# Kernel optimization log

Measured on AMD Instinct MI355X. Metric: run time of the kernel, lower is better.

Reference implementation:

```python
import jax, jax.numpy as jnp
import numpy as np

N = 100000          # nodes
E = 1200000         # edges
IN_DIM = 128
HID = 64
NUM_CLASSES = 5
NUM_GRAPHS = 128


def setup_inputs() -> dict:
    key = jax.random.key(0)
    ks = jax.random.split(key, 12)
    x = jax.random.normal(ks[0], (N, IN_DIM), dtype=jnp.float32)
    edge_index = jax.random.randint(ks[1], (2, E), 0, N, dtype=jnp.int64)
    batch = jnp.sort(jax.random.randint(ks[2], (N,), 0, NUM_GRAPHS, dtype=jnp.int64))
    def glorot(k, shape):
        lim = np.sqrt(6.0 / (shape[0] + shape[1]))
        return jax.random.uniform(k, shape, jnp.float32, -lim, lim)
    W1 = glorot(ks[3], (IN_DIM, HID)); b1 = jnp.zeros((HID,), jnp.float32)
    W2 = glorot(ks[4], (HID, HID));    b2 = jnp.zeros((HID,), jnp.float32)
    W3 = glorot(ks[5], (HID, HID));    b3 = jnp.zeros((HID,), jnp.float32)
    Wc = glorot(ks[6], (HID, NUM_CLASSES)); bc = jnp.zeros((NUM_CLASSES,), jnp.float32)
    return {"x": x, "edge_index": edge_index, "batch": batch,
            "W1": W1, "b1": b1, "W2": W2, "b2": b2, "W3": W3, "b3": b3,
            "Wc": Wc, "bc": bc}


def _gcn_norm(edge_index, n_nodes):
    # PyG GCNConv: add self-loops, symmetric normalization D^-1/2 (A+I) D^-1/2
    loop = jnp.arange(n_nodes, dtype=edge_index.dtype)
    src = jnp.concatenate([edge_index[0], loop])  # [E+N]
    dst = jnp.concatenate([edge_index[1], loop])
    deg = jax.ops.segment_sum(jnp.ones_like(dst, dtype=jnp.float32), dst,
                              num_segments=n_nodes)
    dinv = jnp.where(deg > 0, jax.lax.rsqrt(deg), 0.0)
    norm = dinv[src] * dinv[dst]                   # [E+N]
    return src, dst, norm


def _gcn_conv(x, src, dst, norm, W, b, n_nodes):
    h = x @ W                                      # [N, out]
    msg = h[src] * norm[:, None]                   # gather + scale
    agg = jax.ops.segment_sum(msg, dst, num_segments=n_nodes)  # scatter-add
    return agg + b


def reference(x, edge_index, batch, W1, b1, W2, b2, W3, b3, Wc, bc):
    src, dst, norm = _gcn_norm(edge_index, N)
    h = jax.nn.relu(_gcn_conv(x, src, dst, norm, W1, b1, N))
    h = jax.nn.relu(_gcn_conv(h, src, dst, norm, W2, b2, N))
    h = jax.nn.relu(_gcn_conv(h, src, dst, norm, W3, b3, N))
    # global_mean_pool over batch ids
    sums = jax.ops.segment_sum(h, batch, num_segments=NUM_GRAPHS)
    counts = jax.ops.segment_sum(jnp.ones((N,), jnp.float32), batch,
                                 num_segments=NUM_GRAPHS)
    pooled = sums / jnp.maximum(counts, 1.0)[:, None]  # [G, HID]
    return pooled @ Wc + bc                             # [G, num_classes]
```

## Files before the change

### kernel.cpp

```cpp
#include <hip/hip_runtime.h>
#include <hip/hip_bf16.h>

#define NN 100000
#define NE 1200000
#define IND 128
#define HID 64
#define NC 5
#define NG 128
#define NB 391
#define GB 1172
#define G1 3125

typedef float v2f __attribute__((ext_vector_type(2)));

static __device__ __forceinline__ float bf2f(unsigned short u) {
    union { unsigned int i; float f; } x;
    x.i = (unsigned int)u << 16;
    return x.f;
}
static __device__ __forceinline__ unsigned short f2bf(float f) {
    union { float f; unsigned int i; } x;
    x.f = f;
    unsigned int r = (x.i + 0x7fffu + ((x.i >> 16) & 1u)) >> 16;
    return (unsigned short)r;
}
static __device__ __forceinline__ unsigned short f2fp8x2(float a, float b) {
    int p = __builtin_amdgcn_cvt_pk_fp8_f32(a, b, 0, false);
    return (unsigned short)(p & 0xffff);
}
static __device__ __forceinline__ void fp8acc(unsigned int u, float& a0, float& a1, float& a2, float& a3) {
    v2f lo = __builtin_amdgcn_cvt_pk_f32_fp8(u, false);
    v2f hi = __builtin_amdgcn_cvt_pk_f32_fp8(u, true);
    a0 += lo.x; a1 += lo.y; a2 += hi.x; a3 += hi.y;
}

__global__ __launch_bounds__(256) void k_hist(const int* __restrict__ dst, int* __restrict__ cnt,
                                              int* __restrict__ rank) {
    int e = blockIdx.x * 256 + threadIdx.x;
    if (e < NE) rank[e] = atomicAdd(&cnt[dst[e]], 1);
}

__global__ __launch_bounds__(256) void k_scan1(const int* __restrict__ cnt, int* __restrict__ exc,
                                               int* __restrict__ bsum, float* __restrict__ dinv) {
    __shared__ int lds[256];
    int tid = threadIdx.x;
    int i = blockIdx.x * 256 + tid;
    int v = (i < NN) ? cnt[i] : 0;
    lds[tid] = v;
    __syncthreads();
    for (int off = 1; off < 256; off <<= 1) {
        int t = (tid >= off) ? lds[tid - off] : 0;
        __syncthreads();
        lds[tid] += t;
        __syncthreads();
    }
    if (i < NN) {
        exc[i] = lds[tid] - v;
        dinv[i] = rsqrtf((float)v + 1.0f);
    }
    if (tid == 255) bsum[blockIdx.x] = lds[255];
}

__global__ __launch_bounds__(256) void k_scan23(const int* __restrict__ exc, const int* __restrict__ bsum,
                                                int* __restrict__ row_ptr) {
    __shared__ int lds[256];
    int tid = threadIdx.x;
    int me = blockIdx.x;
    int v = 0;
    if (tid < me) v = bsum[tid];
    if (tid + 256 < me) v += bsum[tid + 256];
    lds[tid] = v;
    __syncthreads();
    for (int off = 128; off > 0; off >>= 1) {
        if (tid < off) lds[tid] += lds[tid + off];
        __syncthreads();
    }
    int base = lds[0];
    int i = me * 256 + tid;
    if (i < NN) row_ptr[i] = exc[i] + base;
    if (i == 0) row_ptr[NN] = NE;
}

__global__ __launch_bounds__(256) void k_fused1(
    const float* __restrict__ X, const float* __restrict__ W,
    const float* __restrict__ dinv, unsigned short* __restrict__ out_f8,
    const int* __restrict__ src, const int* __restrict__ dst,
    const int* __restrict__ row_ptr, const int* __restrict__ rank,
    int* __restrict__ src_sorted,
    const int* __restrict__ batch, int* __restrict__ start)
{
    __shared__ float lds[IND * HID + 32 * IND];
    int tid = threadIdx.x;

    if (blockIdx.x < GB) {
        int t = blockIdx.x * 256 + tid;
        const int T = GB * 256;
#pragma unroll
        for (int u = 0; u < 4; ++u) {
            int e = t + u * T;
            if (e < NE) src_sorted[row_ptr[dst[e]] + rank[e]] = src[e];
        }
        return;
    }
    if (blockIdx.x >= GB + G1) {
        int i = (blockIdx.x - GB - G1) * 256 + tid;
        if (i >= NN) return;
        int b = batch[i];
        if (i == 0) {
            for (int g = 0; g <= b; ++g) start[g] = 0;
        } else {
            int p = batch[i - 1];
            for (int g = p + 1; g <= b; ++g) start[g] = i;
        }
        if (i == NN - 1) {
            for (int g = b + 1; g <= NG; ++g) start[g] = NN;
        }
        return;
    }

    float* Wl = lds;
    float* xl = lds + IND * HID;
    int n0 = (blockIdx.x - GB) * 32;
    int c = tid & 31;
    int s = tid >> 5;

    {
        const float4* Wg = (const float4*)W;
        float4* Wl4 = (float4*)Wl;
#pragma unroll
        for (int i = 0; i < IND * 16 / 256; ++i) Wl4[i * 256 + tid] = Wg[i * 256 + tid];
    }
    {
        const float4* Xg = (const float4*)X;
        float4* xl4 = (float4*)xl;
        const float4 z = {0.f, 0.f, 0.f, 0.f};
#pragma unroll
        for (int i = 0; i < 32 * IND / 4 / 256; ++i) {
            int idx = i * 256 + tid;
            int node = n0 + idx / (IND / 4);
            xl4[idx] = (node < NN) ? Xg[(size_t)n0 * (IND / 4) + idx] : z;
        }
    }
    __syncthreads();

    float acc[4][2];
#pragma unroll
    for (int r = 0; r < 4; ++r) { acc[r][0] = 0.f; acc[r][1] = 0.f; }

#pragma unroll 4
    for (int k0 = 0; k0 < IND; k0 += 4) {
        float4 xv[4];
#pragma unroll
        for (int r = 0; r < 4; ++r) xv[r] = *(const float4*)&xl[(s * 4 + r) * IND + k0];
#pragma unroll
        for (int kk = 0; kk < 4; ++kk) {
            float w0 = Wl[(k0 + kk) * HID + 2 * c];
            float w1 = Wl[(k0 + kk) * HID + 2 * c + 1];
#pragma unroll
            for (int r = 0; r < 4; ++r) {
                float xe = (kk == 0) ? xv[r].x : (kk == 1) ? xv[r].y : (kk == 2) ? xv[r].z : xv[r].w;
                acc[r][0] = fmaf(xe, w0, acc[r][0]);
                acc[r][1] = fmaf(xe, w1, acc[r][1]);
            }
        }
    }

#pragma unroll
    for (int r = 0; r < 4; ++r) {
        int n = n0 + s * 4 + r;
        if (n < NN) {
            float dn = dinv[n];
            out_f8[(size_t)n * 32 + c] = f2fp8x2(acc[r][0] * dn, acc[r][1] * dn);
        }
    }
}

__global__ __launch_bounds__(256) void k_aggregate(const unsigned int* __restrict__ hW8,
                                                   const int* __restrict__ srcs,
                                                   const int* __restrict__ row_ptr,
                                                   const float* __restrict__ dinv,
                                                   const float* __restrict__ b,
                                                   unsigned int* __restrict__ outb) {
    int tid = threadIdx.x;
    int lane = tid & 63;
    int grp = lane >> 4;
    int li = lane & 15;
    int n = blockIdx.x * 4 + (tid >> 6);

    float a0 = 0.f, a1 = 0.f, a2 = 0.f, a3 = 0.f;
    if (grp == 0) {
        unsigned int su = hW8[(size_t)n * 16 + li];
        fp8acc(su, a0, a1, a2, a3);
    }

    int e = row_ptr[n];
    int end = row_ptr[n + 1];

    for (; e + 7 < end; e += 8) {
        int sA = srcs[e + grp];
        int sB = srcs[e + 4 + grp];
        unsigned int uA = hW8[(size_t)sA * 16 + li];
        unsigned int uB = hW8[(size_t)sB * 16 + li];
        fp8acc(uA, a0, a1, a2, a3);
        fp8acc(uB, a0, a1, a2, a3);
    }
    if (e + 3 < end) {
        int sA = srcs[e + grp];
        unsigned int uA = hW8[(size_t)sA * 16 + li];
        fp8acc(uA, a0, a1, a2, a3);
        e += 4;
    }
    int rem = end - e;
    if (grp < rem) {
        int sA = srcs[e + grp];
        unsigned int uA = hW8[(size_t)sA * 16 + li];
        fp8acc(uA, a0, a1, a2, a3);
    }

    a0 += __shfl_xor(a0, 16, 64);
    a1 += __shfl_xor(a1, 16, 64);
    a2 += __shfl_xor(a2, 16, 64);
    a3 += __shfl_xor(a3, 16, 64);
    a0 += __shfl_xor(a0, 32, 64);
    a1 += __shfl_xor(a1, 32, 64);
    a2 += __shfl_xor(a2, 32, 64);
    a3 += __shfl_xor(a3, 32, 64);

    if (lane < 16) {
        float dn = dinv[n];
        float4 bv = ((const float4*)b)[li];
        float v0 = fmaxf(fmaf(dn, a0, bv.x), 0.0f);
        float v1 = fmaxf(fmaf(dn, a1, bv.y), 0.0f);
        float v2 = fmaxf(fmaf(dn, a2, bv.z), 0.0f);
        float v3 = fmaxf(fmaf(dn, a3, bv.w), 0.0f);
        uint2 p;
        p.x = (unsigned int)f2bf(v0) | ((unsigned int)f2bf(v1) << 16);
        p.y = (unsigned int)f2bf(v2) | ((unsigned int)f2bf(v3) << 16);
        ((uint2*)outb)[(size_t)n * 16 + li] = p;
    }
}

__global__ __launch_bounds__(256) void k_gemm_bf(const unsigned short* __restrict__ X,
                                                 const float* __restrict__ W,
                                                 const float* __restrict__ dinv,
                                                 unsigned short* __restrict__ out_f8) {
    __shared__ float Wl[HID * HID];
    __shared__ float xl[64 * HID];
    int tid = threadIdx.x;
    int n0 = blockIdx.x * 64;

    {
        const float4* Wg = (const float4*)W;
        float4* Wl4 = (float4*)Wl;
#pragma unroll
        for (int i = 0; i < HID * HID / 4 / 256; ++i) Wl4[i * 256 + tid] = Wg[i * 256 + tid];
    }
    {
        const uint4* Xg = (const uint4*)X;
#pragma unroll
        for (int i = 0; i < 2; ++i) {
            int idx = i * 256 + tid;
            int ln = idx >> 3;
            int k0 = (idx & 7) * 8;
            int node = n0 + ln;
            float f[8];
            if (node < NN) {
                uint4 u = Xg[(size_t)n0 * 8 + idx];
                f[0] = bf2f((unsigned short)(u.x & 0xffff));
                f[1] = bf2f((unsigned short)(u.x >> 16));
                f[2] = bf2f((unsigned short)(u.y & 0xffff));
                f[3] = bf2f((unsigned short)(u.y >> 16));
                f[4] = bf2f((unsigned short)(u.z & 0xffff));
                f[5] = bf2f((unsigned short)(u.z >> 16));
                f[6] = bf2f((unsigned short)(u.w & 0xffff));
                f[7] = bf2f((unsigned short)(u.w >> 16));
            } else {
#pragma unroll
                for (int q = 0; q < 8; ++q) f[q] = 0.f;
            }
#pragma unroll
            for (int q = 0; q < 8; ++q) xl[ln * HID + k0 + q] = f[q];
        }
    }
    __syncthreads();

    int c = tid & 31;
    int s = tid >> 5;
    float acc[8][2];
#pragma unroll
    for (int r = 0; r < 8; ++r) { acc[r][0] = 0.f; acc[r][1] = 0.f; }

#pragma unroll 4
    for (int k0 = 0; k0 < HID; k0 += 4) {
        float4 xv[8];
#pragma unroll
        for (int r = 0; r < 8; ++r) xv[r] = *(const float4*)&xl[(s * 8 + r) * HID + k0];
#pragma unroll
        for (int kk = 0; kk < 4; ++kk) {
            float w0 = Wl[(k0 + kk) * HID + 2 * c];
            float w1 = Wl[(k0 + kk) * HID + 2 * c + 1];
#pragma unroll
            for (int r = 0; r < 8; ++r) {
                float xe = (kk == 0) ? xv[r].x : (kk == 1) ? xv[r].y : (kk == 2) ? xv[r].z : xv[r].w;
                acc[r][0] = fmaf(xe, w0, acc[r][0]);
                acc[r][1] = fmaf(xe, w1, acc[r][1]);
            }
        }
    }

#pragma unroll
    for (int r = 0; r < 8; ++r) {
        int n = n0 + s * 8 + r;
        if (n < NN) {
            float dn = dinv[n];
            out_f8[(size_t)n * 32 + c] = f2fp8x2(acc[r][0] * dn, acc[r][1] * dn);
        }
    }
}

__global__ __launch_bounds__(256) void k_pool_partial(const unsigned short* __restrict__ h,
                                                      const int* __restrict__ batch,
                                                      float* __restrict__ sums) {
    int tid = threadIdx.x;
    int j = tid & 63;
    int w = tid >> 6;
    int chunk = blockIdx.x * 4 + w;
    int n0 = chunk * 128;
    if (n0 >= NN) return;
    int n1 = n0 + 128;
    if (n1 > NN) n1 = NN;
    float acc = 0.0f;
    int cur = batch[n0];
    for (int n = n0; n < n1; ++n) {
        int g = batch[n];
        if (g != cur) {
            atomicAdd(&sums[cur * HID + j], acc);
            acc = 0.0f;
            cur = g;
        }
        acc += bf2f(h[n * HID + j]);
    }
    atomicAdd(&sums[cur * HID + j], acc);
}

__global__ __launch_bounds__(64) void k_head(const float* __restrict__ sums, const int* __restrict__ start,
                                             const float* __restrict__ Wc, const float* __restrict__ bc,
                                             float* __restrict__ out) {
    int g = blockIdx.x;
    int j = threadIdx.x;
    float cnt = (float)(start[g + 1] - start[g]);
    float p = sums[g * HID + j] / fmaxf(cnt, 1.0f);
#pragma unroll
    for (int c = 0; c < NC; ++c) {
        float v = p * Wc[j * NC + c];
        for (int off = 32; off > 0; off >>= 1) v += __shfl_down(v, off);
        if (j == 0) out[g * NC + c] = v + bc[c];
    }
}

extern "C" void kernel_launch(void* const* d_in, const int* in_sizes, int n_in,
                              void* d_out, int out_size, void* d_ws, size_t ws_size,
                              hipStream_t stream) {
    const float* x  = (const float*)d_in[0];
    const int* ei   = (const int*)d_in[1];
    const int* bat  = (const int*)d_in[2];
    const float* W1 = (const float*)d_in[3];
    const float* b1 = (const float*)d_in[4];
    const float* W2 = (const float*)d_in[5];
    const float* b2 = (const float*)d_in[6];
    const float* W3 = (const float*)d_in[7];
    const float* b3 = (const float*)d_in[8];
    const float* Wc = (const float*)d_in[9];
    const float* bc = (const float*)d_in[10];
    float* out = (float*)d_out;

    const int* src = ei;
    const int* dst = ei + NE;

    char* wsb = (char*)d_ws;
    float* dinv         = (float*)wsb;
    int*   row_ptr      = (int*)(wsb + 400000);
    int*   srcs         = (int*)(wsb + 800016);
    unsigned short* hF8 = (unsigned short*)(wsb + 5600016);
    unsigned short* hBF = (unsigned short*)(wsb + 18400016);
    int*   cnt          = (int*)(wsb + 31200016);
    int*   exc          = (int*)(wsb + 31600016);
    int*   bsum         = (int*)(wsb + 32000016);
    int*   rank         = (int*)(wsb + 32002064);
    int*   start        = (int*)(wsb + 36802064);
    float* sums         = (float*)(wsb + 36803088);

    const int gE = (NE + 255) / 256;

    hipMemsetAsync(cnt, 0, NN * sizeof(int), stream);
    hipMemsetAsync(sums, 0, NG * HID * sizeof(float), stream);
    k_hist<<<gE, 256, 0, stream>>>(dst, cnt, rank);
    k_scan1<<<NB, 256, 0, stream>>>(cnt, exc, bsum, dinv);
    k_scan23<<<NB, 256, 0, stream>>>(exc, bsum, row_ptr);

    k_fused1<<<GB + G1 + NB, 256, 0, stream>>>(x, W1, dinv, hF8, src, dst, row_ptr, rank, srcs, bat, start);

    k_aggregate<<<NN / 4, 256, 0, stream>>>((const unsigned int*)hF8, srcs, row_ptr, dinv, b1, (unsigned int*)hBF);
    k_gemm_bf<<<(NN + 63) / 64, 256, 0, stream>>>(hBF, W2, dinv, hF8);
    k_aggregate<<<NN / 4, 256, 0, stream>>>((const unsigned int*)hF8, srcs, row_ptr, dinv, b2, (unsigned int*)hBF);
    k_gemm_bf<<<(NN + 63) / 64, 256, 0, stream>>>(hBF, W3, dinv, hF8);
    k_aggregate<<<NN / 4, 256, 0, stream>>>((const unsigned int*)hF8, srcs, row_ptr, dinv, b3, (unsigned int*)hBF);

    k_pool_partial<<<196, 256, 0, stream>>>(hBF, bat, sums);
    k_head<<<NG, 64, 0, stream>>>(sums, start, Wc, bc, out);
}
```

Baseline: 338.2 us.

## Process eight nodes per wavefront in aggregation, two interleaved at a time

The aggregation kernel now assigns 8 consecutive destination nodes to each wavefront instead of one. It handles them in pairs with separate accumulators, interleaving the gathers of both nodes so each iteration has two independent loads in flight. Row pointers for all 8 nodes are loaded once and broadcast with shuffles, and the grid shrinks 8x. This aims to amortize per-node setup and raise memory-level parallelism, at the cost of serialization within a wave, uneven tail handling when degrees differ, and fewer resident waves.

```diff
diff --git a/kernel.cpp b/kernel.cpp
--- a/kernel.cpp
+++ b/kernel.cpp
@@ -179,64 +179,95 @@
                                                    const int* __restrict__ srcs,
                                                    const int* __restrict__ row_ptr,
                                                    const float* __restrict__ dinv,
-                                                   const float* __restrict__ b,
+                                                   const float* __restrict__ bias,
                                                    unsigned int* __restrict__ outb) {
     int tid = threadIdx.x;
     int lane = tid & 63;
     int grp = lane >> 4;
     int li = lane & 15;
-    int n = blockIdx.x * 4 + (tid >> 6);
-
-    float a0 = 0.f, a1 = 0.f, a2 = 0.f, a3 = 0.f;
-    if (grp == 0) {
-        unsigned int su = hW8[(size_t)n * 16 + li];
-        fp8acc(su, a0, a1, a2, a3);
-    }
-
-    int e = row_ptr[n];
-    int end = row_ptr[n + 1];
-
-    for (; e + 7 < end; e += 8) {
-        int sA = srcs[e + grp];
-        int sB = srcs[e + 4 + grp];
-        unsigned int uA = hW8[(size_t)sA * 16 + li];
-        unsigned int uB = hW8[(size_t)sB * 16 + li];
-        fp8acc(uA, a0, a1, a2, a3);
-        fp8acc(uB, a0, a1, a2, a3);
-    }
-    if (e + 3 < end) {
-        int sA = srcs[e + grp];
-        unsigned int uA = hW8[(size_t)sA * 16 + li];
-        fp8acc(uA, a0, a1, a2, a3);
-        e += 4;
-    }
-    int rem = end - e;
-    if (grp < rem) {
-        int sA = srcs[e + grp];
-        unsigned int uA = hW8[(size_t)sA * 16 + li];
-        fp8acc(uA, a0, a1, a2, a3);
-    }
-
-    a0 += __shfl_xor(a0, 16, 64);
-    a1 += __shfl_xor(a1, 16, 64);
-    a2 += __shfl_xor(a2, 16, 64);
-    a3 += __shfl_xor(a3, 16, 64);
-    a0 += __shfl_xor(a0, 32, 64);
-    a1 += __shfl_xor(a1, 32, 64);
-    a2 += __shfl_xor(a2, 32, 64);
-    a3 += __shfl_xor(a3, 32, 64);
-
-    if (lane < 16) {
-        float dn = dinv[n];
-        float4 bv = ((const float4*)b)[li];
-        float v0 = fmaxf(fmaf(dn, a0, bv.x), 0.0f);
-        float v1 = fmaxf(fmaf(dn, a1, bv.y), 0.0f);
-        float v2 = fmaxf(fmaf(dn, a2, bv.z), 0.0f);
-        float v3 = fmaxf(fmaf(dn, a3, bv.w), 0.0f);
-        uint2 p;
-        p.x = (unsigned int)f2bf(v0) | ((unsigned int)f2bf(v1) << 16);
-        p.y = (unsigned int)f2bf(v2) | ((unsigned int)f2bf(v3) << 16);
-        ((uint2*)outb)[(size_t)n * 16 + li] = p;
+    int w = tid >> 6;
+    int base = (blockIdx.x * 4 + w) * 8;
+
+    int rp = row_ptr[base + (lane <= 8 ? lane : 8)];
+
+    for (int p = 0; p < 4; ++p) {
+        int nA = base + 2 * p;
+        int nB = nA + 1;
+        int eA = __shfl(rp, 2 * p, 64);
+        int ea = __shfl(rp, 2 * p + 1, 64);
+        int eB = ea;
+        int eb = __shfl(rp, 2 * p + 2, 64);
+
+        float a0 = 0.f, a1 = 0.f, a2 = 0.f, a3 = 0.f;
+        float c0 = 0.f, c1 = 0.f, c2 = 0.f, c3 = 0.f;
+
+        {
+            int sn = (grp & 1) ? nB : nA;
+            unsigned int su = hW8[(size_t)sn * 16 + li];
+            if (grp == 0) fp8acc(su, a0, a1, a2, a3);
+            else if (grp == 1) fp8acc(su, c0, c1, c2, c3);
+        }
+
+        while (eA + 3 < ea && eB + 3 < eb) {
+            int sA = srcs[eA + grp];
+            int sB = srcs[eB + grp];
+            unsigned int uA = hW8[(size_t)sA * 16 + li];
+            unsigned int uB = hW8[(size_t)sB * 16 + li];
+            fp8acc(uA, a0, a1, a2, a3);
+            fp8acc(uB, c0, c1, c2, c3);
+            eA += 4; eB += 4;
+        }
+        while (eA + 3 < ea) {
+            int sA = srcs[eA + grp];
+            unsigned int uA = hW8[(size_t)sA * 16 + li];
+            fp8acc(uA, a0, a1, a2, a3);
+            eA += 4;
+        }
+        while (eB + 3 < eb) {
+            int sB = srcs[eB + grp];
+            unsigned int uB = hW8[(size_t)sB * 16 + li];
+            fp8acc(uB, c0, c1, c2, c3);
+            eB += 4;
+        }
+        int remA = ea - eA;
+        if (grp < remA) {
+            int sA = srcs[eA + grp];
+            unsigned int uA = hW8[(size_t)sA * 16 + li];
+            fp8acc(uA, a0, a1, a2, a3);
+        }
+        int remB = eb - eB;
+        if (grp < remB) {
+            int sB = srcs[eB + grp];
+            unsigned int uB = hW8[(size_t)sB * 16 + li];
+            fp8acc(uB, c0, c1, c2, c3);
+        }
+
+        a0 += __shfl_xor(a0, 16, 64); a1 += __shfl_xor(a1, 16, 64);
+        a2 += __shfl_xor(a2, 16, 64); a3 += __shfl_xor(a3, 16, 64);
+        c0 += __shfl_xor(c0, 16, 64); c1 += __shfl_xor(c1, 16, 64);
+        c2 += __shfl_xor(c2, 16, 64); c3 += __shfl_xor(c3, 16, 64);
+        a0 += __shfl_xor(a0, 32, 64); a1 += __shfl_xor(a1, 32, 64);
+        a2 += __shfl_xor(a2, 32, 64); a3 += __shfl_xor(a3, 32, 64);
+        c0 += __shfl_xor(c0, 32, 64); c1 += __shfl_xor(c1, 32, 64);
+        c2 += __shfl_xor(c2, 32, 64); c3 += __shfl_xor(c3, 32, 64);
+
+        if (grp < 2) {
+            int n = (grp == 0) ? nA : nB;
+            float s0 = (grp == 0) ? a0 : c0;
+            float s1 = (grp == 0) ? a1 : c1;
+            float s2 = (grp == 0) ? a2 : c2;
+            float s3 = (grp == 0) ? a3 : c3;
+            float dn = dinv[n];
+            float4 bv = ((const float4*)bias)[li];
+            float v0 = fmaxf(fmaf(dn, s0, bv.x), 0.0f);
+            float v1 = fmaxf(fmaf(dn, s1, bv.y), 0.0f);
+            float v2 = fmaxf(fmaf(dn, s2, bv.z), 0.0f);
+            float v3 = fmaxf(fmaf(dn, s3, bv.w), 0.0f);
+            uint2 pk;
+            pk.x = (unsigned int)f2bf(v0) | ((unsigned int)f2bf(v1) << 16);
+            pk.y = (unsigned int)f2bf(v2) | ((unsigned int)f2bf(v3) << 16);
+            ((uint2*)outb)[(size_t)n * 16 + li] = pk;
+        }
     }
 }
 
@@ -400,11 +431,11 @@
 
     k_fused1<<<GB + G1 + NB, 256, 0, stream>>>(x, W1, dinv, hF8, src, dst, row_ptr, rank, srcs, bat, start);
 
-    k_aggregate<<<NN / 4, 256, 0, stream>>>((const unsigned int*)hF8, srcs, row_ptr, dinv, b1, (unsigned int*)hBF);
+    k_aggregate<<<NN / 32, 256, 0, stream>>>((const unsigned int*)hF8, srcs, row_ptr, dinv, b1, (unsigned int*)hBF);
     k_gemm_bf<<<(NN + 63) / 64, 256, 0, stream>>>(hBF, W2, dinv, hF8);
-    k_aggregate<<<NN / 4, 256, 0, stream>>>((const unsigned int*)hF8, srcs, row_ptr, dinv, b2, (unsigned int*)hBF);
+    k_aggregate<<<NN / 32, 256, 0, stream>>>((const unsigned int*)hF8, srcs, row_ptr, dinv, b2, (unsigned int*)hBF);
     k_gemm_bf<<<(NN + 63) / 64, 256, 0, stream>>>(hBF, W3, dinv, hF8);
-    k_aggregate<<<NN / 4, 256, 0, stream>>>((const unsigned int*)hF8, srcs, row_ptr, dinv, b3, (unsigned int*)hBF);
+    k_aggregate<<<NN / 32, 256, 0, stream>>>((const unsigned int*)hF8, srcs, row_ptr, dinv, b3, (unsigned int*)hBF);
 
     k_pool_partial<<<196, 256, 0, stream>>>(hBF, bat, sums);
     k_head<<<NG, 64, 0, stream>>>(sums, start, Wc, bc, out);
```

Result: faster. 316.4 us (-6.4%).
